# Kernel optimization log

Hardware: AMD Instinct MI355X
Metric: run time of the kernel (lower is better)

## Reference

```python
import jax, jax.numpy as jnp
import numpy as np

N_NODES = 50000
N_EDGES = 1000000
HIDDEN = 64
NUM_GRAPHS = 512
EPS = 1e-5


def _instance_norm(x, seg, num_graphs):
    # per-graph, per-channel normalization (PyG InstanceNorm, affine=False)
    ones = jnp.ones((x.shape[0], 1), x.dtype)
    cnt = jnp.clip(jax.ops.segment_sum(ones, seg, num_segments=num_graphs), 1.0)
    mean = jax.ops.segment_sum(x, seg, num_segments=num_graphs) / cnt
    xc = x - mean[seg]
    var = jax.ops.segment_sum(xc * xc, seg, num_segments=num_graphs) / cnt
    return xc * jax.lax.rsqrt(var + EPS)[seg]


def setup_inputs() -> dict:
    key = jax.random.key(0)
    ks = jax.random.split(key, 10)
    emb = jax.random.normal(ks[0], (N_NODES, HIDDEN), jnp.float32)
    edge_index = jax.random.randint(ks[1], (2, N_EDGES), 0, N_NODES, jnp.int64 if jax.config.read('jax_enable_x64') else jnp.int32)
    batch = jnp.sort(jax.random.randint(ks[2], (N_NODES,), 0, NUM_GRAPHS))
    h = HIDDEN
    # channels = [2h, 4h, h, 1]
    W1 = jax.random.normal(ks[3], (2 * h, 4 * h), jnp.float32) * 0.05
    b1 = jnp.zeros((4 * h,), jnp.float32)
    W2 = jax.random.normal(ks[4], (4 * h, h), jnp.float32) * 0.05
    b2 = jnp.zeros((h,), jnp.float32)
    W3 = jax.random.normal(ks[5], (h, 1), jnp.float32) * 0.05
    b3 = jnp.zeros((1,), jnp.float32)
    return {"emb": emb, "W1": W1, "b1": b1, "W2": W2, "b2": b2,
            "W3": W3, "b3": b3, "edge_index": edge_index, "batch": batch}


def reference(emb, W1, b1, W2, b2, W3, b3, edge_index, batch):
    col, row = edge_index[0], edge_index[1]
    f12 = jnp.concatenate([emb[col], emb[row]], axis=-1)  # [E, 2h]
    seg = batch[col]  # per-edge graph id
    x = f12 @ W1 + b1                                      # [E, 4h]
    x = jax.nn.relu(_instance_norm(x, seg, NUM_GRAPHS))
    x = x @ W2 + b2                                        # [E, h]
    x = jax.nn.relu(_instance_norm(x, seg, NUM_GRAPHS))
    return x @ W3 + b3                                     # [E, 1]
```

## Files before the change

kernel.cpp:

```cpp
#include <hip/hip_runtime.h>
#include <hip/hip_bf16.h>

#define EDGES 1000000
#define NNODES 50000
#define NG 512
#define NTILES 15625
#define NCOLB 50176

typedef __attribute__((ext_vector_type(8))) short bf16x8;
typedef __attribute__((ext_vector_type(4))) float f32x4;

__device__ __forceinline__ unsigned short f2bf(float f){
  unsigned u = __float_as_uint(f);
  u += 0x7fffu + ((u >> 16) & 1u);
  return (unsigned short)(u >> 16);
}
__device__ __forceinline__ float bf2f(unsigned short h){
  return __uint_as_float(((unsigned)h) << 16);
}
__device__ __forceinline__ unsigned pk2bf(float x, float y){
  __hip_bfloat162 h = __float22bfloat162_rn(make_float2(x, y));
  union { __hip_bfloat162 h; unsigned u; } cv; cv.h = h;
  return cv.u;
}

__global__ void prep_all(const float* __restrict__ emb, const float* __restrict__ W1,
                         const float* __restrict__ W2,
                         unsigned short* __restrict__ emb_bf,
                         unsigned short* __restrict__ w1tn, unsigned short* __restrict__ w2t){
  int i = blockIdx.x * 256 + threadIdx.x;
  if (i < NNODES * 64){
    emb_bf[i] = f2bf(emb[i]);
  } else {
    int j = i - NNODES * 64;
    if (j < 32768){
      int jj = j >> 6, k = j & 63;
      float v = (jj < 256) ? W1[k * 256 + jj] : W1[(k + 64) * 256 + (jj - 256)];
      w1tn[j] = f2bf(v);
    } else {
      int jj = j - 32768;
      if (jj < 16384){
        int n = jj >> 8, k = jj & 255;
        w2t[jj] = f2bf(W2[k * 64 + n]);
      }
    }
  }
}

__global__ void seg_hist(const int* __restrict__ ei, const int* __restrict__ batch,
                         unsigned* __restrict__ hist){
  __shared__ unsigned h[NG];
  int t = threadIdx.x;
  h[t] = 0; h[t + 256] = 0;
  __syncthreads();
  for (int i = 0; i < 4; i++){
    int e = blockIdx.x * 1024 + i * 256 + t;
    if (e < EDGES){
      int s = batch[ei[e]];
      atomicAdd(&h[s], 1u);
    }
  }
  __syncthreads();
  atomicAdd(&hist[t], h[t]);
  atomicAdd(&hist[t + 256], h[t + 256]);
}

__global__ void col_hist(const int* __restrict__ ei, unsigned* __restrict__ chist){
  for (int i = 0; i < 4; i++){
    int e = blockIdx.x * 1024 + i * 256 + threadIdx.x;
    if (e < EDGES) atomicAdd(&chist[ei[e]], 1u);
  }
}

__global__ void col_scan1(const unsigned* __restrict__ chist, unsigned* __restrict__ cpre,
                          unsigned* __restrict__ bsum){
  __shared__ unsigned s[256];
  int t = threadIdx.x;
  int i = blockIdx.x * 256 + t;
  unsigned v = (i < NNODES) ? chist[i] : 0u;
  s[t] = v;
  __syncthreads();
  for (int o = 1; o < 256; o <<= 1){
    unsigned u = (t >= o) ? s[t - o] : 0u;
    __syncthreads();
    s[t] += u;
    __syncthreads();
  }
  cpre[i] = s[t] - v;
  if (t == 255) bsum[blockIdx.x] = s[255];
}

__global__ void col_scan2(unsigned* __restrict__ bsum){
  __shared__ unsigned s[256];
  int t = threadIdx.x;
  unsigned v = (t < 196) ? bsum[t] : 0u;
  s[t] = v;
  __syncthreads();
  for (int o = 1; o < 256; o <<= 1){
    unsigned u = (t >= o) ? s[t - o] : 0u;
    __syncthreads();
    s[t] += u;
    __syncthreads();
  }
  if (t < 196) bsum[t] = s[t] - v;
}

__global__ void col_scan3(unsigned* __restrict__ cpre, const unsigned* __restrict__ bsum){
  int i = blockIdx.x * 256 + threadIdx.x;
  cpre[i] += bsum[blockIdx.x];
}

__global__ void col_scatter(const int* __restrict__ ei, const int* __restrict__ batch,
                            unsigned* __restrict__ cpre, int4* __restrict__ emeta){
  for (int i = 0; i < 4; i++){
    int e = blockIdx.x * 1024 + i * 256 + threadIdx.x;
    if (e < EDGES){
      int cn = ei[e];
      int pos = (int)atomicAdd(&cpre[cn], 1u);
      emeta[pos] = make_int4(cn, ei[EDGES + e], batch[cn], e);
    }
  }
}

__global__ __launch_bounds__(256) void node_gemm(
    const unsigned short* __restrict__ emb_bf, const unsigned short* __restrict__ w1tn,
    unsigned short* __restrict__ P)
{
  __shared__ unsigned short As[64 * 72];
  int t = threadIdx.x;
  int n0 = blockIdx.x * 64;
  {
    int nl = t >> 2, part = t & 3;
    int node = n0 + nl; if (node >= NNODES) node = 0;
    const int4* src = (const int4*)(emb_bf + node * 64 + part * 16);
    int4* dst = (int4*)(As + nl * 72 + part * 16);
    dst[0] = src[0]; dst[1] = src[1];
  }
  __syncthreads();
  int w = t >> 6, lane = t & 63, q = lane >> 4, c = lane & 15;
  f32x4 acc[4][8];
  for (int a = 0; a < 4; a++) for (int b = 0; b < 8; b++) for (int r = 0; r < 4; r++) acc[a][b][r] = 0.f;
  for (int k0 = 0; k0 < 64; k0 += 32){
    bf16x8 af[4];
    for (int tt = 0; tt < 4; tt++) af[tt] = *(const bf16x8*)(As + (tt * 16 + c) * 72 + k0 + q * 8);
    for (int n4 = 0; n4 < 8; n4++){
      bf16x8 bw = *(const bf16x8*)(w1tn + (w * 128 + n4 * 16 + c) * 64 + k0 + q * 8);
      for (int tt = 0; tt < 4; tt++)
        acc[tt][n4] = __builtin_amdgcn_mfma_f32_16x16x32_bf16(af[tt], bw, acc[tt][n4], 0, 0, 0);
    }
  }
  for (int tt = 0; tt < 4; tt++){
    for (int r = 0; r < 4; r++){
      int node = n0 + tt * 16 + q * 4 + r;
      if (node < NNODES){
        unsigned short* dst = P + (size_t)node * 512 + w * 128 + c;
        for (int n4 = 0; n4 < 8; n4++) dst[n4 * 16] = f2bf(acc[tt][n4][r]);
      }
    }
  }
}

__global__ __launch_bounds__(256) void k1_gather(
    const unsigned short* __restrict__ P, const int4* __restrict__ emeta,
    float* __restrict__ sum1, float* __restrict__ sqs1)
{
  int lane = threadIdx.x & 63;
  int wid = (blockIdx.x * 256 + threadIdx.x) >> 6;
  if (wid >= NTILES) return;
  int p0 = wid * 64;
  int4 me = emeta[p0 + lane];
  int c4 = lane * 4;
  int s0 = __builtin_amdgcn_readlane(me.z, 0);
  bool uni = (__ballot(me.z == s0) == ~0ull);
  float sm0 = 0.f, sm1 = 0.f, sm2 = 0.f, sm3 = 0.f;
  float q0 = 0.f, q1 = 0.f, q2 = 0.f, q3 = 0.f;
  if (uni){
    int cprev = -1;
    ushort4 a = make_ushort4(0,0,0,0);
    int re = __builtin_amdgcn_readlane(me.y, 0);
    ushort4 b = *(const ushort4*)(P + (size_t)re * 512 + 256 + c4);
    #pragma unroll 4
    for (int e = 0; e < 64; e++){
      ushort4 bn = b;
      if (e < 63){
        int rn = __builtin_amdgcn_readlane(me.y, e + 1);
        bn = *(const ushort4*)(P + (size_t)rn * 512 + 256 + c4);
      }
      int ce = __builtin_amdgcn_readlane(me.x, e);
      if (ce != cprev){ a = *(const ushort4*)(P + (size_t)ce * 512 + c4); cprev = ce; }
      float x0 = bf2f(a.x) + bf2f(b.x);
      float x1 = bf2f(a.y) + bf2f(b.y);
      float x2v = bf2f(a.z) + bf2f(b.z);
      float x3 = bf2f(a.w) + bf2f(b.w);
      sm0 += x0; q0 += x0 * x0;
      sm1 += x1; q1 += x1 * x1;
      sm2 += x2v; q2 += x2v * x2v;
      sm3 += x3; q3 += x3 * x3;
      b = bn;
    }
    float* sp = sum1 + s0 * 256 + c4;
    float* qp = sqs1 + s0 * 256 + c4;
    atomicAdd(sp + 0, sm0); atomicAdd(sp + 1, sm1); atomicAdd(sp + 2, sm2); atomicAdd(sp + 3, sm3);
    atomicAdd(qp + 0, q0);  atomicAdd(qp + 1, q1);  atomicAdd(qp + 2, q2);  atomicAdd(qp + 3, q3);
  } else {
    int cur = s0;
    int cprev = -1;
    ushort4 a = make_ushort4(0,0,0,0);
    for (int e = 0; e < 64; e++){
      int ce = __builtin_amdgcn_readlane(me.x, e);
      int re = __builtin_amdgcn_readlane(me.y, e);
      if (ce != cprev){ a = *(const ushort4*)(P + (size_t)ce * 512 + c4); cprev = ce; }
      ushort4 b = *(const ushort4*)(P + (size_t)re * 512 + 256 + c4);
      int s = __builtin_amdgcn_readlane(me.z, e);
      if (s != cur){
        float* sp = sum1 + cur * 256 + c4;
        float* qp = sqs1 + cur * 256 + c4;
        atomicAdd(sp + 0, sm0); atomicAdd(sp + 1, sm1); atomicAdd(sp + 2, sm2); atomicAdd(sp + 3, sm3);
        atomicAdd(qp + 0, q0);  atomicAdd(qp + 1, q1);  atomicAdd(qp + 2, q2);  atomicAdd(qp + 3, q3);
        sm0 = sm1 = sm2 = sm3 = 0.f; q0 = q1 = q2 = q3 = 0.f;
        cur = s;
      }
      float x0 = bf2f(a.x) + bf2f(b.x);
      float x1 = bf2f(a.y) + bf2f(b.y);
      float x2v = bf2f(a.z) + bf2f(b.z);
      float x3 = bf2f(a.w) + bf2f(b.w);
      sm0 += x0; q0 += x0 * x0;
      sm1 += x1; q1 += x1 * x1;
      sm2 += x2v; q2 += x2v * x2v;
      sm3 += x3; q3 += x3 * x3;
    }
    float* sp = sum1 + cur * 256 + c4;
    float* qp = sqs1 + cur * 256 + c4;
    atomicAdd(sp + 0, sm0); atomicAdd(sp + 1, sm1); atomicAdd(sp + 2, sm2); atomicAdd(sp + 3, sm3);
    atomicAdd(qp + 0, q0);  atomicAdd(qp + 1, q1);  atomicAdd(qp + 2, q2);  atomicAdd(qp + 3, q3);
  }
}

__global__ void finalize1(const float* __restrict__ sum1, const float* __restrict__ sqs1,
                          const unsigned* __restrict__ hist, float* __restrict__ r1,
                          float* __restrict__ mr1){
  int i = blockIdx.x * 256 + threadIdx.x;
  int g = i >> 8;
  float cnt = fmaxf((float)hist[g], 1.f);
  float m = sum1[i] / cnt;
  float v = sqs1[i] / cnt - m * m;
  v = fmaxf(v, 0.f);
  float r = rsqrtf(v + 1e-5f);
  r1[i] = r;
  mr1[i] = m * r;
}

__global__ void finalize2(const float* __restrict__ sum2, const float* __restrict__ sqs2,
                          const unsigned* __restrict__ hist, float* __restrict__ r2,
                          float* __restrict__ mr2){
  int i = blockIdx.x * 256 + threadIdx.x;
  int g = i >> 6;
  float cnt = fmaxf((float)hist[g], 1.f);
  float m = sum2[i] / cnt;
  float v = sqs2[i] / cnt - m * m;
  v = fmaxf(v, 0.f);
  float r = rsqrtf(v + 1e-5f);
  r2[i] = r;
  mr2[i] = m * r;
}

__global__ __launch_bounds__(256) void k2_fused(
    const unsigned short* __restrict__ P, const unsigned short* __restrict__ w2t,
    const int4* __restrict__ emeta,
    const float* __restrict__ r1, const float* __restrict__ mr1,
    float* __restrict__ sum2, float* __restrict__ sqs2,
    unsigned short* __restrict__ x2t)
{
  __shared__ unsigned short Y[64 * 264];
  __shared__ int segl[64];
  __shared__ short rsegA[64];
  __shared__ unsigned char rloA[65];
  __shared__ int nrunS;
  int t = threadIdx.x;
  int p0 = blockIdx.x * 64;
  int w = t >> 6, lane = t & 63, q = lane >> 4, c = lane & 15;
  if (t < 64) segl[t] = emeta[p0 + t].z;
  if (w == 0){
    int sN = segl[lane];
    int nxt = (lane < 63) ? segl[lane + 1] : sN;
    unsigned long long mask = __ballot(sN != nxt);
    if (lane == 0){
      if (mask == 0ull){
        nrunS = 1; rloA[0] = 0; rloA[1] = 64; rsegA[0] = (short)sN;
      } else {
        int n = 0, cur = segl[0];
        rsegA[0] = (short)cur; rloA[0] = 0;
        for (int i = 1; i < 64; i++)
          if (segl[i] != cur){ cur = segl[i]; n++; rsegA[n] = (short)cur; rloA[n] = (unsigned char)i; }
        rloA[n + 1] = 64; nrunS = n + 1;
      }
    }
  }
  int c4 = lane * 4;
  int elb0 = w * 16;
  int4 me = emeta[p0 + elb0 + (lane & 15)];
  __syncthreads();
  int nrun = nrunS;
  bool uni = (nrun == 1);

  float4 r4, mr4;
  if (uni){
    int s0 = segl[0];
    r4  = *(const float4*)(r1  + s0 * 256 + c4);
    mr4 = *(const float4*)(mr1 + s0 * 256 + c4);
  }
  {
    int cprev = -1;
    ushort4 a = make_ushort4(0,0,0,0);
    int re = __builtin_amdgcn_readlane(me.y, 0);
    ushort4 b = *(const ushort4*)(P + (size_t)re * 512 + 256 + c4);
    for (int e = 0; e < 16; e++){
      ushort4 bn = b;
      if (e < 15){
        int rn = __builtin_amdgcn_readlane(me.y, e + 1);
        bn = *(const ushort4*)(P + (size_t)rn * 512 + 256 + c4);
      }
      int ce = __builtin_amdgcn_readlane(me.x, e);
      if (ce != cprev){ a = *(const ushort4*)(P + (size_t)ce * 512 + c4); cprev = ce; }
      if (!uni){
        int s = __builtin_amdgcn_readlane(me.z, e);
        r4  = *(const float4*)(r1  + s * 256 + c4);
        mr4 = *(const float4*)(mr1 + s * 256 + c4);
      }
      float y0 = fmaxf(0.f, (bf2f(a.x) + bf2f(b.x)) * r4.x - mr4.x);
      float y1 = fmaxf(0.f, (bf2f(a.y) + bf2f(b.y)) * r4.y - mr4.y);
      float y2 = fmaxf(0.f, (bf2f(a.z) + bf2f(b.z)) * r4.z - mr4.z);
      float y3 = fmaxf(0.f, (bf2f(a.w) + bf2f(b.w)) * r4.w - mr4.w);
      uint2 pk;
      pk.x = pk2bf(y0, y1);
      pk.y = pk2bf(y2, y3);
      *(uint2*)(Y + (elb0 + e) * 264 + c4) = pk;
      b = bn;
    }
  }
  __syncthreads();

  f32x4 acc2[4];
  for (int tt = 0; tt < 4; tt++) for (int r = 0; r < 4; r++) acc2[tt][r] = 0.f;
  int ch2 = w * 16 + c;
  for (int kc = 0; kc < 8; kc++){
    int k0 = kc * 32;
    bf16x8 bfr = *(const bf16x8*)(w2t + ch2 * 256 + k0 + q * 8);
    for (int tt = 0; tt < 4; tt++){
      bf16x8 afr = *(const bf16x8*)(Y + (tt * 16 + c) * 264 + k0 + q * 8);
      acc2[tt] = __builtin_amdgcn_mfma_f32_16x16x32_bf16(afr, bfr, acc2[tt], 0, 0, 0);
    }
  }

  if (uni){
    int s = segl[0];
    float sm = 0.f, sq = 0.f;
    for (int tt = 0; tt < 4; tt++)
      for (int r = 0; r < 4; r++){
        float v = acc2[tt][r];
        sm += v; sq += v * v;
      }
    sm += __shfl_xor(sm, 16); sq += __shfl_xor(sq, 16);
    sm += __shfl_xor(sm, 32); sq += __shfl_xor(sq, 32);
    if (q == 0){
      atomicAdd(&sum2[s * 64 + ch2], sm);
      atomicAdd(&sqs2[s * 64 + ch2], sq);
    }
  } else {
    for (int rr = 0; rr < nrun; rr++){
      int s = rsegA[rr], lo = rloA[rr], hi = rloA[rr + 1];
      float sm = 0.f, sq = 0.f;
      for (int tt = 0; tt < 4; tt++){
        int elb = tt * 16 + q * 4;
        for (int r = 0; r < 4; r++){
          int el = elb + r;
          if (el >= lo && el < hi){
            float v = acc2[tt][r];
            sm += v; sq += v * v;
          }
        }
      }
      sm += __shfl_xor(sm, 16); sq += __shfl_xor(sq, 16);
      sm += __shfl_xor(sm, 32); sq += __shfl_xor(sq, 32);
      if (q == 0){
        atomicAdd(&sum2[s * 64 + ch2], sm);
        atomicAdd(&sqs2[s * 64 + ch2], sq);
      }
    }
  }
  for (int tt = 0; tt < 4; tt++){
    uint2 pk;
    pk.x = pk2bf(acc2[tt][0], acc2[tt][1]);
    pk.y = pk2bf(acc2[tt][2], acc2[tt][3]);
    *(uint2*)(x2t + (size_t)ch2 * EDGES + p0 + tt * 16 + q * 4) = pk;
  }
}

__global__ __launch_bounds__(256) void k3_out(
    const unsigned short* __restrict__ x2t, const int4* __restrict__ emeta,
    const float* __restrict__ r2, const float* __restrict__ mr2,
    const float* __restrict__ W3, const float* __restrict__ b3, float* __restrict__ out)
{
  int pp = blockIdx.x * 256 + threadIdx.x;
  if (pp >= EDGES) return;
  int4 me = emeta[pp];
  const float* r2p  = r2  + me.z * 64;
  const float* mr2p = mr2 + me.z * 64;
  float acc = 0.f;
  #pragma unroll 8
  for (int ch = 0; ch < 64; ch++){
    float v = bf2f(x2t[(size_t)ch * EDGES + pp]);
    float y = fmaxf(0.f, v * r2p[ch] - mr2p[ch]);
    acc += y * W3[ch];
  }
  out[me.w] = acc + b3[0];
}

extern "C" void kernel_launch(void* const* d_in, const int* in_sizes, int n_in,
                              void* d_out, int out_size, void* d_ws, size_t ws_size,
                              hipStream_t stream)
{
  (void)in_sizes; (void)n_in; (void)out_size;
  const float* emb = (const float*)d_in[0];
  const float* W1  = (const float*)d_in[1];
  const float* W2  = (const float*)d_in[3];
  const float* W3  = (const float*)d_in[5];
  const float* b3  = (const float*)d_in[6];
  const int* ei    = (const int*)d_in[7];
  const int* batch = (const int*)d_in[8];
  float* out = (float*)d_out;

  char* p = (char*)d_ws;
  size_t off = 0;
  auto take = [&](size_t n) -> char* {
    char* r = p + off;
    off += (n + 255) & ~(size_t)255;
    return r;
  };

  unsigned short* emb_bf = (unsigned short*)take((size_t)NNODES * 64 * 2);
  unsigned short* w1tn   = (unsigned short*)take(32768 * 2);
  unsigned short* w2t    = (unsigned short*)take(16384 * 2);
  int4* emeta = (int4*)take((size_t)EDGES * 16);
  unsigned short* P   = (unsigned short*)take((size_t)NNODES * 512 * 2);
  unsigned short* x2t = (unsigned short*)take((size_t)EDGES * 64 * 2);
  float* r1  = (float*)take(512 * 256 * 4);
  float* mr1 = (float*)take(512 * 256 * 4);
  float* r2  = (float*)take(512 * 64 * 4);
  float* mr2 = (float*)take(512 * 64 * 4);
  unsigned* cpre = (unsigned*)take(NCOLB * 4);
  unsigned* bsum = (unsigned*)take(256 * 4);
  char* zbase = p + off;
  unsigned* hist  = (unsigned*)take(NG * 4);
  unsigned* chist = (unsigned*)take(NCOLB * 4);
  float* sum1 = (float*)take(512 * 256 * 4);
  float* sqs1 = (float*)take(512 * 256 * 4);
  float* sum2 = (float*)take(512 * 64 * 4);
  float* sqs2 = (float*)take(512 * 64 * 4);
  size_t zsize = (size_t)((p + off) - zbase);

  if (ws_size < off) return;

  hipMemsetAsync(zbase, 0, zsize, stream);
  prep_all<<<12692, 256, 0, stream>>>(emb, W1, W2, emb_bf, w1tn, w2t);
  seg_hist<<<977, 256, 0, stream>>>(ei, batch, hist);
  col_hist<<<977, 256, 0, stream>>>(ei, chist);
  col_scan1<<<196, 256, 0, stream>>>(chist, cpre, bsum);
  col_scan2<<<1, 256, 0, stream>>>(bsum);
  col_scan3<<<196, 256, 0, stream>>>(cpre, bsum);
  col_scatter<<<977, 256, 0, stream>>>(ei, batch, cpre, emeta);
  node_gemm<<<(NNODES + 63) / 64, 256, 0, stream>>>(emb_bf, w1tn, P);
  k1_gather<<<(NTILES + 3) / 4, 256, 0, stream>>>(P, emeta, sum1, sqs1);
  finalize1<<<512, 256, 0, stream>>>(sum1, sqs1, hist, r1, mr1);
  k2_fused<<<NTILES, 256, 0, stream>>>(P, w2t, emeta, r1, mr1, sum2, sqs2, x2t);
  finalize2<<<128, 256, 0, stream>>>(sum2, sqs2, hist, r2, mr2);
  k3_out<<<3907, 256, 0, stream>>>(x2t, emeta, r2, mr2, W3, b3, out);
}
```

Measured before the change: 592.9 us.

## Batch row gathers for memory-level parallelism and add XCD block swizzle

Result: slower. 715.6 us (+20.7%).

```diff
diff --git a/kernel.cpp b/kernel.cpp
--- a/kernel.cpp
+++ b/kernel.cpp
@@ -22,6 +22,12 @@
   __hip_bfloat162 h = __float22bfloat162_rn(make_float2(x, y));
   union { __hip_bfloat162 h; unsigned u; } cv; cv.h = h;
   return cv.u;
+}
+__device__ __forceinline__ int xcd_swizzle(int bid, int nb){
+  int nb8 = nb & ~7;
+  if (bid >= nb8) return bid;
+  int per = nb8 >> 3;
+  return (bid & 7) * per + (bid >> 3);
 }
 
 __global__ void prep_all(const float* __restrict__ emb, const float* __restrict__ W1,
@@ -165,7 +171,8 @@
     float* __restrict__ sum1, float* __restrict__ sqs1)
 {
   int lane = threadIdx.x & 63;
-  int wid = (blockIdx.x * 256 + threadIdx.x) >> 6;
+  int bid = xcd_swizzle(blockIdx.x, gridDim.x);
+  int wid = (bid * 256 + threadIdx.x) >> 6;
   if (wid >= NTILES) return;
   int p0 = wid * 64;
   int4 me = emeta[p0 + lane];
@@ -175,28 +182,29 @@
   float sm0 = 0.f, sm1 = 0.f, sm2 = 0.f, sm3 = 0.f;
   float q0 = 0.f, q1 = 0.f, q2 = 0.f, q3 = 0.f;
   if (uni){
-    int cprev = -1;
-    ushort4 a = make_ushort4(0,0,0,0);
-    int re = __builtin_amdgcn_readlane(me.y, 0);
-    ushort4 b = *(const ushort4*)(P + (size_t)re * 512 + 256 + c4);
-    #pragma unroll 4
-    for (int e = 0; e < 64; e++){
-      ushort4 bn = b;
-      if (e < 63){
-        int rn = __builtin_amdgcn_readlane(me.y, e + 1);
-        bn = *(const ushort4*)(P + (size_t)rn * 512 + 256 + c4);
-      }
-      int ce = __builtin_amdgcn_readlane(me.x, e);
-      if (ce != cprev){ a = *(const ushort4*)(P + (size_t)ce * 512 + c4); cprev = ce; }
-      float x0 = bf2f(a.x) + bf2f(b.x);
-      float x1 = bf2f(a.y) + bf2f(b.y);
-      float x2v = bf2f(a.z) + bf2f(b.z);
-      float x3 = bf2f(a.w) + bf2f(b.w);
-      sm0 += x0; q0 += x0 * x0;
-      sm1 += x1; q1 += x1 * x1;
-      sm2 += x2v; q2 += x2v * x2v;
-      sm3 += x3; q3 += x3 * x3;
-      b = bn;
+    int cprev = __builtin_amdgcn_readlane(me.x, 0);
+    ushort4 a = *(const ushort4*)(P + (size_t)cprev * 512 + c4);
+    #pragma unroll
+    for (int eb = 0; eb < 64; eb += 16){
+      ushort4 bb[16];
+      #pragma unroll
+      for (int j = 0; j < 16; j++){
+        int re = __builtin_amdgcn_readlane(me.y, eb + j);
+        bb[j] = *(const ushort4*)(P + (size_t)re * 512 + 256 + c4);
+      }
+      #pragma unroll
+      for (int j = 0; j < 16; j++){
+        int ce = __builtin_amdgcn_readlane(me.x, eb + j);
+        if (ce != cprev){ a = *(const ushort4*)(P + (size_t)ce * 512 + c4); cprev = ce; }
+        float x0 = bf2f(a.x) + bf2f(bb[j].x);
+        float x1 = bf2f(a.y) + bf2f(bb[j].y);
+        float x2v = bf2f(a.z) + bf2f(bb[j].z);
+        float x3 = bf2f(a.w) + bf2f(bb[j].w);
+        sm0 += x0; q0 += x0 * x0;
+        sm1 += x1; q1 += x1 * x1;
+        sm2 += x2v; q2 += x2v * x2v;
+        sm3 += x3; q3 += x3 * x3;
+      }
     }
     float* sp = sum1 + s0 * 256 + c4;
     float* qp = sqs1 + s0 * 256 + c4;
@@ -277,8 +285,25 @@
   __shared__ unsigned char rloA[65];
   __shared__ int nrunS;
   int t = threadIdx.x;
-  int p0 = blockIdx.x * 64;
+  int bid = xcd_swizzle(blockIdx.x, gridDim.x);
+  int p0 = bid * 64;
   int w = t >> 6, lane = t & 63, q = lane >> 4, c = lane & 15;
+  int c4 = lane * 4;
+  int elb0 = w * 16;
+  int4 me = emeta[p0 + elb0 + (lane & 15)];
+
+  ushort4 bb[16];
+  #pragma unroll
+  for (int e = 0; e < 16; e++){
+    int re = __builtin_amdgcn_readlane(me.y, e);
+    bb[e] = *(const ushort4*)(P + (size_t)re * 512 + 256 + c4);
+  }
+  int cprev = __builtin_amdgcn_readlane(me.x, 0);
+  ushort4 a = *(const ushort4*)(P + (size_t)cprev * 512 + c4);
+  int s0g = __builtin_amdgcn_readlane(me.z, 0);
+  float4 r4  = *(const float4*)(r1  + s0g * 256 + c4);
+  float4 mr4 = *(const float4*)(mr1 + s0g * 256 + c4);
+
   if (t < 64) segl[t] = emeta[p0 + t].z;
   if (w == 0){
     int sN = segl[lane];
@@ -296,47 +321,28 @@
       }
     }
   }
-  int c4 = lane * 4;
-  int elb0 = w * 16;
-  int4 me = emeta[p0 + elb0 + (lane & 15)];
   __syncthreads();
   int nrun = nrunS;
   bool uni = (nrun == 1);
 
-  float4 r4, mr4;
-  if (uni){
-    int s0 = segl[0];
-    r4  = *(const float4*)(r1  + s0 * 256 + c4);
-    mr4 = *(const float4*)(mr1 + s0 * 256 + c4);
-  }
-  {
-    int cprev = -1;
-    ushort4 a = make_ushort4(0,0,0,0);
-    int re = __builtin_amdgcn_readlane(me.y, 0);
-    ushort4 b = *(const ushort4*)(P + (size_t)re * 512 + 256 + c4);
-    for (int e = 0; e < 16; e++){
-      ushort4 bn = b;
-      if (e < 15){
-        int rn = __builtin_amdgcn_readlane(me.y, e + 1);
-        bn = *(const ushort4*)(P + (size_t)rn * 512 + 256 + c4);
-      }
-      int ce = __builtin_amdgcn_readlane(me.x, e);
-      if (ce != cprev){ a = *(const ushort4*)(P + (size_t)ce * 512 + c4); cprev = ce; }
-      if (!uni){
-        int s = __builtin_amdgcn_readlane(me.z, e);
-        r4  = *(const float4*)(r1  + s * 256 + c4);
-        mr4 = *(const float4*)(mr1 + s * 256 + c4);
-      }
-      float y0 = fmaxf(0.f, (bf2f(a.x) + bf2f(b.x)) * r4.x - mr4.x);
-      float y1 = fmaxf(0.f, (bf2f(a.y) + bf2f(b.y)) * r4.y - mr4.y);
-      float y2 = fmaxf(0.f, (bf2f(a.z) + bf2f(b.z)) * r4.z - mr4.z);
-      float y3 = fmaxf(0.f, (bf2f(a.w) + bf2f(b.w)) * r4.w - mr4.w);
-      uint2 pk;
-      pk.x = pk2bf(y0, y1);
-      pk.y = pk2bf(y2, y3);
-      *(uint2*)(Y + (elb0 + e) * 264 + c4) = pk;
-      b = bn;
-    }
+  #pragma unroll
+  for (int e = 0; e < 16; e++){
+    int ce = __builtin_amdgcn_readlane(me.x, e);
+    if (ce != cprev){ a = *(const ushort4*)(P + (size_t)ce * 512 + c4); cprev = ce; }
+    float4 rr4 = r4, mm4 = mr4;
+    if (!uni){
+      int s = __builtin_amdgcn_readlane(me.z, e);
+      rr4 = *(const float4*)(r1  + s * 256 + c4);
+      mm4 = *(const float4*)(mr1 + s * 256 + c4);
+    }
+    float y0 = fmaxf(0.f, (bf2f(a.x) + bf2f(bb[e].x)) * rr4.x - mm4.x);
+    float y1 = fmaxf(0.f, (bf2f(a.y) + bf2f(bb[e].y)) * rr4.y - mm4.y);
+    float y2 = fmaxf(0.f, (bf2f(a.z) + bf2f(bb[e].z)) * rr4.z - mm4.z);
+    float y3 = fmaxf(0.f, (bf2f(a.w) + bf2f(bb[e].w)) * rr4.w - mm4.w);
+    uint2 pk;
+    pk.x = pk2bf(y0, y1);
+    pk.y = pk2bf(y2, y3);
+    *(uint2*)(Y + (elb0 + e) * 264 + c4) = pk;
   }
   __syncthreads();
 
```
